# Performance work log

Hardware: AMD Instinct MI355X
Metric: run time of the kernel (lower is better)

## Reference

```python
import jax, jax.numpy as jnp
import numpy as np

N = 40000   # num nodes (== in_channels, featureless RGCN)
E = 640000  # num edges
R = 8       # num relations
H = 128     # hidden channels
C = 64      # out channels


def setup_inputs() -> dict:
    key = jax.random.key(0)
    k = jax.random.split(key, 8)
    edge_index = jax.random.randint(k[0], (2, E), 0, N)
    edge_type = jax.random.randint(k[1], (E,), 0, R)
    s1 = 1.0 / np.sqrt(N)
    s2 = 1.0 / np.sqrt(H)
    W1 = jax.random.normal(k[2], (R, N, H), jnp.float32) * s1
    root1 = jax.random.normal(k[3], (N, H), jnp.float32) * s1
    b1 = jnp.zeros((H,), jnp.float32)
    W2 = jax.random.normal(k[4], (R, H, C), jnp.float32) * s2
    root2 = jax.random.normal(k[5], (H, C), jnp.float32) * s2
    b2 = jnp.zeros((C,), jnp.float32)
    return {"edge_index": edge_index, "edge_type": edge_type,
            "W1": W1, "root1": root1, "b1": b1,
            "W2": W2, "root2": root2, "b2": b2}


def _segment_mean_per_relation(msg, dst, etype, n_nodes, n_rel):
    # mean aggregation per (destination node, relation), then sum over relations
    seg = dst * n_rel + etype                      # [E]
    sums = jax.ops.segment_sum(msg, seg, num_segments=n_nodes * n_rel)
    cnt = jax.ops.segment_sum(jnp.ones((msg.shape[0], 1), msg.dtype), seg,
                              num_segments=n_nodes * n_rel)
    mean = sums / jnp.maximum(cnt, 1.0)            # [N*R, F]
    return mean.reshape(n_nodes, n_rel, -1).sum(axis=1)  # [N, F]


def reference(edge_index, edge_type, W1, root1, b1, W2, root2, b2):
    src, dst = edge_index[0], edge_index[1]
    # ---- conv1 (x=None): message = W1[rel] row of the source node ----
    msg1 = W1[edge_type, src]                      # [E, H] gather
    h = _segment_mean_per_relation(msg1, dst, edge_type, N, R)
    h = h + root1 + b1                             # root weight acts as embedding
    h = jax.nn.relu(h)
    # ---- conv2: per-relation dense transform then gather per edge ----
    h_all = jnp.einsum('nh,rhc->rnc', h, W2)       # [R, N, C]
    msg2 = h_all[edge_type, src]                   # [E, C]
    out = _segment_mean_per_relation(msg2, dst, edge_type, N, R)
    out = out + h @ root2 + b2                     # [N, C]
    return out
```

## Files before the change

### kernel.cpp

```cpp
#include <hip/hip_runtime.h>

#define N_NODES 40000
#define N_EDGES 640000
#define N_REL   8
#define H_DIM   128
#define C_DIM   64
#define NR      (N_NODES * N_REL)
#define SCAN_ITEMS 40

typedef __attribute__((ext_vector_type(8))) short bf16x8;
typedef __attribute__((ext_vector_type(4))) float f32x4;

__device__ inline uint rne_bf16(float x) {
    uint u = __float_as_uint(x);
    return (u + 0x7FFFu + ((u >> 16) & 1u)) >> 16;
}
__device__ inline uint pack_bf16(float x, float y) {
    return rne_bf16(x) | (rne_bf16(y) << 16);
}
__device__ inline float bf_lo(uint v) { return __uint_as_float(v << 16); }
__device__ inline float bf_hi(uint v) { return __uint_as_float(v & 0xFFFF0000u); }

__global__ void count_kernel(const int* __restrict__ ei,
                             const int* __restrict__ et,
                             int* __restrict__ cnt, int* __restrict__ deg) {
    int e = blockIdx.x * blockDim.x + threadIdx.x;
    if (e < N_EDGES) {
        int dst = ei[N_EDGES + e];
        atomicAdd(&cnt[dst * N_REL + et[e]], 1);
        atomicAdd(&deg[dst], 1);
    }
}

__global__ __launch_bounds__(1024) void
scan_all(const int* __restrict__ deg, int* __restrict__ start) {
    __shared__ int lds[1024];
    int t = threadIdx.x;
    int v[SCAN_ITEMS]; int s = 0;
    #pragma unroll
    for (int j = 0; j < SCAN_ITEMS; j++) {
        int idx = t * SCAN_ITEMS + j;
        v[j] = (idx < N_NODES) ? deg[idx] : 0;
        s += v[j];
    }
    lds[t] = s; __syncthreads();
    int x = s;
    for (int off = 1; off < 1024; off <<= 1) {
        int y = (t >= off) ? lds[t - off] : 0;
        __syncthreads();
        x += y; lds[t] = x;
        __syncthreads();
    }
    int excl = x - s;
    #pragma unroll
    for (int j = 0; j < SCAN_ITEMS; j++) {
        int idx = t * SCAN_ITEMS + j;
        if (idx < N_NODES) start[idx] = excl;
        excl += v[j];
    }
    if (t == 1023) start[N_NODES] = x;
}

__global__ void reorder_kernel(const int* __restrict__ ei, const int* __restrict__ et,
                               const int* __restrict__ start, const int* __restrict__ cnt,
                               int* __restrict__ cursor, int2* __restrict__ em) {
    int e = blockIdx.x * blockDim.x + threadIdx.x;
    if (e < N_EDGES) {
        int r = et[e];
        int dst = ei[N_EDGES + e];
        int pos = atomicAdd(&cursor[dst], 1);
        em[start[dst] + pos] =
            make_int2(ei[e] | (r << 16),
                      __float_as_int(1.0f / (float)cnt[dst * N_REL + r]));
    }
}

__global__ void convert_w2(const float* __restrict__ W2, const float* __restrict__ root2,
                           ushort* __restrict__ w2t) {
    int i = blockIdx.x * 256 + threadIdx.x;
    if (i >= 9 * C_DIM * H_DIM) return;
    int k = i & 127; int c = (i >> 7) & 63; int r = i >> 13;
    float v = (r < 8) ? W2[((size_t)r * H_DIM + k) * C_DIM + c]
                      : root2[(size_t)k * C_DIM + c];
    int byte = (c * 256 + k * 2) ^ ((c & 7) << 4);
    w2t[(size_t)r * 8192 + (byte >> 1)] = (ushort)rne_bf16(v);
}

__global__ __launch_bounds__(256) void
conv1_gather(const int2* __restrict__ em, const int* __restrict__ start,
             const float* __restrict__ W1, const float* __restrict__ root1,
             const float* __restrict__ b1, uint* __restrict__ h16) {
    int lane = threadIdx.x & 63, wv = threadIdx.x >> 6;
    int eg = lane >> 5, q = lane & 31;
    int n = blockIdx.x * 4 + wv;
    int e0 = start[n], e1 = start[n + 1];
    float4 acc = make_float4(0.f, 0.f, 0.f, 0.f);
    for (int base = e0; base < e1; base += 64) {
        int m = e1 - base; if (m > 64) m = 64;
        int2 md = make_int2(0, 0);
        if (lane < m) md = em[base + lane];
        int i = 0;
        for (; i + 8 <= m; i += 8) {
            int i0 = i + eg, i1 = i + eg + 2, i2 = i + eg + 4, i3 = i + eg + 6;
            int p0 = __shfl(md.x, i0), p1 = __shfl(md.x, i1);
            int p2 = __shfl(md.x, i2), p3 = __shfl(md.x, i3);
            float w0 = __int_as_float(__shfl(md.y, i0));
            float w1 = __int_as_float(__shfl(md.y, i1));
            float w2 = __int_as_float(__shfl(md.y, i2));
            float w3 = __int_as_float(__shfl(md.y, i3));
            float4 v0 = ((const float4*)(W1 + ((size_t)(p0 >> 16) * N_NODES + (p0 & 0xFFFF)) * H_DIM))[q];
            float4 v1 = ((const float4*)(W1 + ((size_t)(p1 >> 16) * N_NODES + (p1 & 0xFFFF)) * H_DIM))[q];
            float4 v2 = ((const float4*)(W1 + ((size_t)(p2 >> 16) * N_NODES + (p2 & 0xFFFF)) * H_DIM))[q];
            float4 v3 = ((const float4*)(W1 + ((size_t)(p3 >> 16) * N_NODES + (p3 & 0xFFFF)) * H_DIM))[q];
            acc.x += w0 * v0.x + w1 * v1.x + w2 * v2.x + w3 * v3.x;
            acc.y += w0 * v0.y + w1 * v1.y + w2 * v2.y + w3 * v3.y;
            acc.z += w0 * v0.z + w1 * v1.z + w2 * v2.z + w3 * v3.z;
            acc.w += w0 * v0.w + w1 * v1.w + w2 * v2.w + w3 * v3.w;
        }
        for (; i < m; i += 2) {
            int ii = i + eg;
            int srcl = (ii < m) ? ii : 0;
            int p = __shfl(md.x, srcl);
            float w = __int_as_float(__shfl(md.y, srcl));
            if (ii < m) {
                float4 v = ((const float4*)(W1 + ((size_t)(p >> 16) * N_NODES + (p & 0xFFFF)) * H_DIM))[q];
                acc.x += w * v.x; acc.y += w * v.y;
                acc.z += w * v.z; acc.w += w * v.w;
            }
        }
    }
    acc.x += __shfl_xor(acc.x, 32);
    acc.y += __shfl_xor(acc.y, 32);
    acc.z += __shfl_xor(acc.z, 32);
    acc.w += __shfl_xor(acc.w, 32);
    if (eg == 0) {
        float4 rt = ((const float4*)root1)[(size_t)n * 32 + q];
        float4 bb = ((const float4*)b1)[q];
        float cx = fmaxf(acc.x + rt.x + bb.x, 0.f);
        float cy = fmaxf(acc.y + rt.y + bb.y, 0.f);
        float cz = fmaxf(acc.z + rt.z + bb.z, 0.f);
        float cw = fmaxf(acc.w + rt.w + bb.w, 0.f);
        uint2 o; o.x = pack_bf16(cx, cy); o.y = pack_bf16(cz, cw);
        ((uint2*)h16)[(size_t)n * 32 + q] = o;
    }
}

__global__ __launch_bounds__(256) void
zgemm(const uint* __restrict__ h16, const ushort* __restrict__ w2t,
      const float* __restrict__ b2, ushort* __restrict__ zb, float* __restrict__ out) {
    __shared__ uint ldsA[4096];
    __shared__ uint ldsB[4096];
    int t = threadIdx.x, lane = t & 63, wv = t >> 6;
    int nbase = blockIdx.x * 64;
    for (int i = t; i < 4096; i += 256) {
        int row = i >> 6, cu = i & 63;
        int byte = (row * 256 + cu * 4) ^ ((row & 7) << 4);
        ldsA[byte >> 2] = h16[(size_t)(nbase + row) * 64 + cu];
    }
    const char* pA = (const char*)ldsA;
    const char* pB = (const char*)ldsB;
    int arow = wv * 16 + (lane & 15);
    int qk = (lane >> 4) * 16;
    for (int rr = 0; rr < 9; rr++) {
        __syncthreads();
        const uint4* bsrc = (const uint4*)(w2t + (size_t)rr * 8192);
        ((uint4*)ldsB)[t]       = bsrc[t];
        ((uint4*)ldsB)[t + 256] = bsrc[t + 256];
        ((uint4*)ldsB)[t + 512] = bsrc[t + 512];
        ((uint4*)ldsB)[t + 768] = bsrc[t + 768];
        __syncthreads();
        f32x4 acc[4];
        #pragma unroll
        for (int ct = 0; ct < 4; ct++) acc[ct] = (f32x4){0.f, 0.f, 0.f, 0.f};
        #pragma unroll
        for (int ct = 0; ct < 4; ct++) {
            int bcol = ct * 16 + (lane & 15);
            #pragma unroll
            for (int kf = 0; kf < 4; kf++) {
                int abyte = (arow * 256 + kf * 64 + qk) ^ ((arow & 7) << 4);
                int bbyte = (bcol * 256 + kf * 64 + qk) ^ ((bcol & 7) << 4);
                bf16x8 a = *(const bf16x8*)(pA + abyte);
                bf16x8 b = *(const bf16x8*)(pB + bbyte);
                acc[ct] = __builtin_amdgcn_mfma_f32_16x16x32_bf16(a, b, acc[ct], 0, 0, 0);
            }
        }
        #pragma unroll
        for (int ct = 0; ct < 4; ct++) {
            int c = ct * 16 + (lane & 15);
            #pragma unroll
            for (int j = 0; j < 4; j++) {
                int n = nbase + wv * 16 + (lane >> 4) * 4 + j;
                if (rr < 8)
                    zb[((size_t)rr * N_NODES + n) * 64 + c] = (ushort)rne_bf16(acc[ct][j]);
                else
                    out[(size_t)n * 64 + c] = acc[ct][j] + b2[c];
            }
        }
    }
}

__global__ __launch_bounds__(256) void
zgather(const int2* __restrict__ em, const int* __restrict__ start,
        const uint* __restrict__ zb32, float* __restrict__ out) {
    int lane = threadIdx.x & 63, wv = threadIdx.x >> 6;
    int n = blockIdx.x * 4 + wv;
    int eg = lane >> 5, c2 = lane & 31;
    int e0 = start[n], e1 = start[n + 1];
    float ax = 0.f, ay = 0.f;
    for (int base = e0; base < e1; base += 64) {
        int m = e1 - base; if (m > 64) m = 64;
        int2 md = make_int2(0, 0);
        if (lane < m) md = em[base + lane];
        int i = 0;
        for (; i + 16 <= m; i += 16) {
            #pragma unroll
            for (int u = 0; u < 2; u++) {
                int j0 = i + u * 8 + eg, j1 = j0 + 2, j2 = j0 + 4, j3 = j0 + 6;
                int p0 = __shfl(md.x, j0), p1 = __shfl(md.x, j1);
                int p2 = __shfl(md.x, j2), p3 = __shfl(md.x, j3);
                float w0 = __int_as_float(__shfl(md.y, j0));
                float w1 = __int_as_float(__shfl(md.y, j1));
                float w2 = __int_as_float(__shfl(md.y, j2));
                float w3 = __int_as_float(__shfl(md.y, j3));
                uint z0 = zb32[((size_t)(p0 >> 16) * N_NODES + (p0 & 0xFFFF)) * 32 + c2];
                uint z1 = zb32[((size_t)(p1 >> 16) * N_NODES + (p1 & 0xFFFF)) * 32 + c2];
                uint z2 = zb32[((size_t)(p2 >> 16) * N_NODES + (p2 & 0xFFFF)) * 32 + c2];
                uint z3 = zb32[((size_t)(p3 >> 16) * N_NODES + (p3 & 0xFFFF)) * 32 + c2];
                ax += w0 * bf_lo(z0) + w1 * bf_lo(z1) + w2 * bf_lo(z2) + w3 * bf_lo(z3);
                ay += w0 * bf_hi(z0) + w1 * bf_hi(z1) + w2 * bf_hi(z2) + w3 * bf_hi(z3);
            }
        }
        for (; i + 8 <= m; i += 8) {
            int j0 = i + eg, j1 = j0 + 2, j2 = j0 + 4, j3 = j0 + 6;
            int p0 = __shfl(md.x, j0), p1 = __shfl(md.x, j1);
            int p2 = __shfl(md.x, j2), p3 = __shfl(md.x, j3);
            float w0 = __int_as_float(__shfl(md.y, j0));
            float w1 = __int_as_float(__shfl(md.y, j1));
            float w2 = __int_as_float(__shfl(md.y, j2));
            float w3 = __int_as_float(__shfl(md.y, j3));
            uint z0 = zb32[((size_t)(p0 >> 16) * N_NODES + (p0 & 0xFFFF)) * 32 + c2];
            uint z1 = zb32[((size_t)(p1 >> 16) * N_NODES + (p1 & 0xFFFF)) * 32 + c2];
            uint z2 = zb32[((size_t)(p2 >> 16) * N_NODES + (p2 & 0xFFFF)) * 32 + c2];
            uint z3 = zb32[((size_t)(p3 >> 16) * N_NODES + (p3 & 0xFFFF)) * 32 + c2];
            ax += w0 * bf_lo(z0) + w1 * bf_lo(z1) + w2 * bf_lo(z2) + w3 * bf_lo(z3);
            ay += w0 * bf_hi(z0) + w1 * bf_hi(z1) + w2 * bf_hi(z2) + w3 * bf_hi(z3);
        }
        for (; i < m; i += 2) {
            int ii = i + eg;
            int srcl = (ii < m) ? ii : 0;
            int p = __shfl(md.x, srcl);
            float w = __int_as_float(__shfl(md.y, srcl));
            if (ii < m) {
                uint zv = zb32[((size_t)(p >> 16) * N_NODES + (p & 0xFFFF)) * 32 + c2];
                ax += w * bf_lo(zv);
                ay += w * bf_hi(zv);
            }
        }
    }
    ax += __shfl_xor(ax, 32);
    ay += __shfl_xor(ay, 32);
    if (eg == 0) {
        float2* o = (float2*)out + (size_t)n * 32 + c2;
        float2 v = *o;
        v.x += ax; v.y += ay;
        *o = v;
    }
}

extern "C" void kernel_launch(void* const* d_in, const int* in_sizes, int n_in,
                              void* d_out, int out_size, void* d_ws, size_t ws_size,
                              hipStream_t stream) {
    const int*   ei    = (const int*)d_in[0];
    const int*   et    = (const int*)d_in[1];
    const float* W1    = (const float*)d_in[2];
    const float* root1 = (const float*)d_in[3];
    const float* b1    = (const float*)d_in[4];
    const float* W2    = (const float*)d_in[5];
    const float* root2 = (const float*)d_in[6];
    const float* b2    = (const float*)d_in[7];
    float* out = (float*)d_out;

    int*    cnt    = (int*)d_ws;
    int*    deg    = cnt + NR;
    int*    cursor = deg + N_NODES;
    int*    start  = cursor + N_NODES;
    int2*   em     = (int2*)(start + N_NODES + 16);
    uint*   h16    = (uint*)(em + N_EDGES);
    ushort* w2t    = (ushort*)(h16 + (size_t)N_NODES * 64);
    ushort* zb     = w2t + 9 * 8192;

    hipMemsetAsync(cnt, 0, (size_t)(NR + 2 * N_NODES) * sizeof(int), stream);

    count_kernel  <<<(N_EDGES + 255) / 256, 256, 0, stream>>>(ei, et, cnt, deg);
    convert_w2    <<<(9 * C_DIM * H_DIM + 255) / 256, 256, 0, stream>>>(W2, root2, w2t);
    scan_all      <<<1, 1024, 0, stream>>>(deg, start);
    reorder_kernel<<<(N_EDGES + 255) / 256, 256, 0, stream>>>(ei, et, start, cnt, cursor, em);
    conv1_gather  <<<N_NODES / 4, 256, 0, stream>>>(em, start, W1, root1, b1, h16);
    zgemm         <<<N_NODES / 64, 256, 0, stream>>>(h16, w2t, b2, zb, out);
    zgather       <<<N_NODES / 4, 256, 0, stream>>>(em, start, (const uint*)zb, out);
}
```

Before: 442.9 us.

## Sort edges by (dst, relation) segment using atomic ranks and multi-block scan

Replaces the per-node degree count, single-block scan and atomic-cursor reorder with a per-(node, relation) count that records each edge's rank, a three-kernel multi-block scan over all N*R segments, and a deterministic scatter with no atomics. Edges are now grouped by relation within each destination, which may improve gather locality, and the second atomic pass is removed. In exchange it adds two kernel launches and a rank array, and scans 320K entries instead of 40K.

```diff
diff --git a/kernel.cpp b/kernel.cpp
--- a/kernel.cpp
+++ b/kernel.cpp
@@ -6,7 +6,7 @@
 #define H_DIM   128
 #define C_DIM   64
 #define NR      (N_NODES * N_REL)
-#define SCAN_ITEMS 40
+#define SCAN_NB ((NR + 1023) / 1024)
 
 typedef __attribute__((ext_vector_type(8))) short bf16x8;
 typedef __attribute__((ext_vector_type(4))) float f32x4;
@@ -21,31 +21,31 @@
 __device__ inline float bf_lo(uint v) { return __uint_as_float(v << 16); }
 __device__ inline float bf_hi(uint v) { return __uint_as_float(v & 0xFFFF0000u); }
 
-__global__ void count_kernel(const int* __restrict__ ei,
-                             const int* __restrict__ et,
-                             int* __restrict__ cnt, int* __restrict__ deg) {
+__global__ void count_rank(const int* __restrict__ ei, const int* __restrict__ et,
+                           int* __restrict__ cnt, int* __restrict__ rank) {
     int e = blockIdx.x * blockDim.x + threadIdx.x;
     if (e < N_EDGES) {
-        int dst = ei[N_EDGES + e];
-        atomicAdd(&cnt[dst * N_REL + et[e]], 1);
-        atomicAdd(&deg[dst], 1);
-    }
-}
-
-__global__ __launch_bounds__(1024) void
-scan_all(const int* __restrict__ deg, int* __restrict__ start) {
-    __shared__ int lds[1024];
+        int seg = ei[N_EDGES + e] * N_REL + et[e];
+        rank[e] = atomicAdd(&cnt[seg], 1);
+    }
+}
+
+__global__ void scanA(const int* __restrict__ cnt, int* __restrict__ segbase,
+                      int* __restrict__ bsum) {
+    __shared__ int lds[256];
+    int base = blockIdx.x * 1024;
     int t = threadIdx.x;
-    int v[SCAN_ITEMS]; int s = 0;
+    int v[4]; int s = 0;
     #pragma unroll
-    for (int j = 0; j < SCAN_ITEMS; j++) {
-        int idx = t * SCAN_ITEMS + j;
-        v[j] = (idx < N_NODES) ? deg[idx] : 0;
+    for (int j = 0; j < 4; j++) {
+        int idx = base + t * 4 + j;
+        v[j] = (idx < NR) ? cnt[idx] : 0;
         s += v[j];
     }
     lds[t] = s; __syncthreads();
     int x = s;
-    for (int off = 1; off < 1024; off <<= 1) {
+    #pragma unroll
+    for (int off = 1; off < 256; off <<= 1) {
         int y = (t >= off) ? lds[t - off] : 0;
         __syncthreads();
         x += y; lds[t] = x;
@@ -53,25 +53,46 @@
     }
     int excl = x - s;
     #pragma unroll
-    for (int j = 0; j < SCAN_ITEMS; j++) {
-        int idx = t * SCAN_ITEMS + j;
-        if (idx < N_NODES) start[idx] = excl;
+    for (int j = 0; j < 4; j++) {
+        int idx = base + t * 4 + j;
+        if (idx < NR) segbase[idx] = excl;
         excl += v[j];
     }
-    if (t == 1023) start[N_NODES] = x;
-}
-
-__global__ void reorder_kernel(const int* __restrict__ ei, const int* __restrict__ et,
-                               const int* __restrict__ start, const int* __restrict__ cnt,
-                               int* __restrict__ cursor, int2* __restrict__ em) {
+    if (t == 255) bsum[blockIdx.x] = x;
+}
+
+__global__ __launch_bounds__(512) void
+scanB(int* __restrict__ bsum, int* __restrict__ segbase) {
+    __shared__ int lds[512];
+    int t = threadIdx.x;
+    int v = (t < SCAN_NB) ? bsum[t] : 0;
+    lds[t] = v; __syncthreads();
+    int x = v;
+    for (int off = 1; off < 512; off <<= 1) {
+        int y = (t >= off) ? lds[t - off] : 0;
+        __syncthreads();
+        x += y; lds[t] = x;
+        __syncthreads();
+    }
+    if (t < SCAN_NB) bsum[t] = x - v;
+    if (t == 511) segbase[NR] = x;
+}
+
+__global__ void scanC(int* __restrict__ segbase, const int* __restrict__ bsum) {
+    int idx = blockIdx.x * blockDim.x + threadIdx.x;
+    if (idx < NR) segbase[idx] += bsum[idx >> 10];
+}
+
+__global__ void scatter_kernel(const int* __restrict__ ei, const int* __restrict__ et,
+                               const int* __restrict__ segbase, const int* __restrict__ cnt,
+                               const int* __restrict__ rank, int2* __restrict__ em) {
     int e = blockIdx.x * blockDim.x + threadIdx.x;
     if (e < N_EDGES) {
         int r = et[e];
-        int dst = ei[N_EDGES + e];
-        int pos = atomicAdd(&cursor[dst], 1);
-        em[start[dst] + pos] =
-            make_int2(ei[e] | (r << 16),
-                      __float_as_int(1.0f / (float)cnt[dst * N_REL + r]));
+        int seg = ei[N_EDGES + e] * N_REL + r;
+        int o = segbase[seg] + rank[e];
+        em[o] = make_int2(ei[e] | (r << 16),
+                          __float_as_int(1.0f / (float)cnt[seg]));
     }
 }
 
@@ -87,13 +108,13 @@
 }
 
 __global__ __launch_bounds__(256) void
-conv1_gather(const int2* __restrict__ em, const int* __restrict__ start,
+conv1_gather(const int2* __restrict__ em, const int* __restrict__ segbase,
              const float* __restrict__ W1, const float* __restrict__ root1,
              const float* __restrict__ b1, uint* __restrict__ h16) {
     int lane = threadIdx.x & 63, wv = threadIdx.x >> 6;
     int eg = lane >> 5, q = lane & 31;
     int n = blockIdx.x * 4 + wv;
-    int e0 = start[n], e1 = start[n + 1];
+    int e0 = segbase[n * N_REL], e1 = segbase[n * N_REL + N_REL];
     float4 acc = make_float4(0.f, 0.f, 0.f, 0.f);
     for (int base = e0; base < e1; base += 64) {
         int m = e1 - base; if (m > 64) m = 64;
@@ -200,12 +221,12 @@
 }
 
 __global__ __launch_bounds__(256) void
-zgather(const int2* __restrict__ em, const int* __restrict__ start,
+zgather(const int2* __restrict__ em, const int* __restrict__ segbase,
         const uint* __restrict__ zb32, float* __restrict__ out) {
     int lane = threadIdx.x & 63, wv = threadIdx.x >> 6;
     int n = blockIdx.x * 4 + wv;
     int eg = lane >> 5, c2 = lane & 31;
-    int e0 = start[n], e1 = start[n + 1];
+    int e0 = segbase[n * N_REL], e1 = segbase[n * N_REL + N_REL];
     float ax = 0.f, ay = 0.f;
     for (int base = e0; base < e1; base += 64) {
         int m = e1 - base; if (m > 64) m = 64;
@@ -280,22 +301,24 @@
     const float* b2    = (const float*)d_in[7];
     float* out = (float*)d_out;
 
-    int*    cnt    = (int*)d_ws;
-    int*    deg    = cnt + NR;
-    int*    cursor = deg + N_NODES;
-    int*    start  = cursor + N_NODES;
-    int2*   em     = (int2*)(start + N_NODES + 16);
-    uint*   h16    = (uint*)(em + N_EDGES);
-    ushort* w2t    = (ushort*)(h16 + (size_t)N_NODES * 64);
-    ushort* zb     = w2t + 9 * 8192;
-
-    hipMemsetAsync(cnt, 0, (size_t)(NR + 2 * N_NODES) * sizeof(int), stream);
-
-    count_kernel  <<<(N_EDGES + 255) / 256, 256, 0, stream>>>(ei, et, cnt, deg);
+    int*    cnt     = (int*)d_ws;
+    int*    segbase = cnt + NR;
+    int*    bsum    = segbase + NR + 16;
+    int*    rank    = bsum + 512;
+    int2*   em      = (int2*)(rank + N_EDGES);
+    uint*   h16     = (uint*)(em + N_EDGES);
+    ushort* w2t     = (ushort*)(h16 + (size_t)N_NODES * 64);
+    ushort* zb      = w2t + 9 * 8192;
+
+    hipMemsetAsync(cnt, 0, (size_t)NR * sizeof(int), stream);
+
+    count_rank    <<<(N_EDGES + 255) / 256, 256, 0, stream>>>(ei, et, cnt, rank);
     convert_w2    <<<(9 * C_DIM * H_DIM + 255) / 256, 256, 0, stream>>>(W2, root2, w2t);
-    scan_all      <<<1, 1024, 0, stream>>>(deg, start);
-    reorder_kernel<<<(N_EDGES + 255) / 256, 256, 0, stream>>>(ei, et, start, cnt, cursor, em);
-    conv1_gather  <<<N_NODES / 4, 256, 0, stream>>>(em, start, W1, root1, b1, h16);
+    scanA         <<<SCAN_NB, 256, 0, stream>>>(cnt, segbase, bsum);
+    scanB         <<<1, 512, 0, stream>>>(bsum, segbase);
+    scanC         <<<(NR + 255) / 256, 256, 0, stream>>>(segbase, bsum);
+    scatter_kernel<<<(N_EDGES + 255) / 256, 256, 0, stream>>>(ei, et, segbase, cnt, rank, em);
+    conv1_gather  <<<N_NODES / 4, 256, 0, stream>>>(em, segbase, W1, root1, b1, h16);
     zgemm         <<<N_NODES / 64, 256, 0, stream>>>(h16, w2t, b2, zb, out);
-    zgather       <<<N_NODES / 4, 256, 0, stream>>>(em, start, (const uint*)zb, out);
-}
+    zgather       <<<N_NODES / 4, 256, 0, stream>>>(em, segbase, (const uint*)zb, out);
+}
```

Result: faster. 369.6 us (-16.6%).
